# Kernel tuning notes

Hardware: AMD Instinct MI355X
Metric: run time of the kernel (lower is better)

The kernel has to match this reference:

```python
import jax, jax.numpy as jnp
import numpy as np

D_MODEL = 2048
D_FFN = 8192
RANK = 16
MOD_SCALE = 0.1
EPS = 1e-6


def setup_inputs() -> dict:
    key = jax.random.key(0)
    ks = jax.random.split(key, 8)
    B, S = 2, 2048
    init_scale = 0.01
    return {
        'hidden_states': jax.random.normal(ks[0], (B, S, D_MODEL), jnp.float32),
        'attn_output': jax.random.normal(ks[1], (B, S, D_MODEL), jnp.float32),
        'A': jax.random.normal(ks[2], (D_MODEL, RANK), jnp.float32) * (init_scale / np.sqrt(D_MODEL)),
        'Bmat': jax.random.normal(ks[3], (RANK, D_FFN), jnp.float32) * (init_scale / np.sqrt(RANK)),
        'W_in': jax.random.normal(ks[4], (D_FFN, D_MODEL), jnp.float32) * 0.02,  # gate_proj.weight
        'W_up': jax.random.normal(ks[5], (D_FFN, D_MODEL), jnp.float32) * 0.02,  # up_proj.weight
        'W_down': jax.random.normal(ks[6], (D_MODEL, D_FFN), jnp.float32) * 0.02,  # down_proj.weight
        'gamma': jnp.ones((D_MODEL,), jnp.float32),  # post_attention_layernorm (RMSNorm) weight
    }


def _rmsnorm(x, gamma):
    var = jnp.mean(x * x, axis=-1, keepdims=True)
    return x * jax.lax.rsqrt(var + EPS) * gamma


def reference(hidden_states, attn_output, A, Bmat, W_in, W_up, W_down, gamma):
    residual = hidden_states
    # Neuro-plastic modulation: [B,S,r]
    modulation = MOD_SCALE * jnp.tanh(jnp.einsum('bsd,dr->bsr', attn_output, A))
    # NPT applies post-attn norm to the residual (not residual+attn)
    h = _rmsnorm(residual, gamma)  # [B,S,d_model]
    # Fused per-token weight delta: delta_w^T @ h == B^T ((A^T h) * mod)
    hA = jnp.einsum('bsd,dr->bsr', h, A)  # [B,S,r]
    delta_out = jnp.einsum('bsr,rf->bsf', hA * modulation, Bmat)  # [B,S,d_ffn]
    gate = jax.nn.silu(jnp.einsum('bsd,fd->bsf', h, W_in) + delta_out)
    up = jnp.einsum('bsd,fd->bsf', h, W_up)
    out = jnp.einsum('bsf,df->bsd', gate * up, W_down)
    return residual + out
```

## Files before the change

kernel.cpp:

```cpp
#include <hip/hip_runtime.h>
#include <cstdint>
#include <cstddef>

#define D_MODEL 2048
#define D_FFN   8192
#define RANK    16
#define EPS     1e-6f
#define MOD_SCALE 0.1f

typedef float    f32x4 __attribute__((ext_vector_type(4)));
typedef _Float16 half8 __attribute__((ext_vector_type(8)));
typedef _Float16 half4 __attribute__((ext_vector_type(4)));

__device__ __forceinline__ void async_load16(const void* g, void* l) {
  __builtin_amdgcn_global_load_lds(
      (const __attribute__((address_space(1))) uint32_t*)g,
      (__attribute__((address_space(3))) uint32_t*)l,
      16, 0, 0);
}

__device__ __forceinline__ void stage_tile(const _Float16* __restrict__ gbase,
                                           size_t stride, _Float16* lds, int tid) {
  #pragma unroll
  for (int j = 0; j < 4; ++j) {
    int idx = j * 256 + tid;
    int row = idx >> 3;
    int c   = (idx & 7) ^ (row & 7);
    async_load16(gbase + (size_t)row * stride + c * 8, &lds[idx * 8]);
  }
}

__device__ __forceinline__ half8 frag_read(const _Float16* lds, int r, int c) {
  return *(const half8*)&lds[r * 64 + ((c ^ (r & 7)) * 8)];
}

__global__ __launch_bounds__(256) void convert_f32_f16(
    const float* __restrict__ s, _Float16* __restrict__ d)
{
  size_t i = ((size_t)blockIdx.x * 256 + threadIdx.x) * 8;
  f32x4 a = *(const f32x4*)(s + i);
  f32x4 b = *(const f32x4*)(s + i + 4);
  half8 h;
  #pragma unroll
  for (int j = 0; j < 4; ++j) { h[j] = (_Float16)a[j]; h[4+j] = (_Float16)b[j]; }
  *(half8*)(d + i) = h;
}

__global__ __launch_bounds__(256) void prep_kernel(
    const float* __restrict__ hs, const float* __restrict__ attn,
    const float* __restrict__ Amat, const float* __restrict__ gamma,
    _Float16* __restrict__ h16, float* __restrict__ cmat)
{
  const int token = blockIdx.x;
  const int tid   = threadIdx.x;
  const int lane  = tid & 63;
  const int wv    = tid >> 6;
  const size_t tb = (size_t)token * D_MODEL;
  const int base  = tid * 8;

  f32x4 x0 = *(const f32x4*)(hs + tb + base);
  f32x4 x1 = *(const f32x4*)(hs + tb + base + 4);
  f32x4 a0 = *(const f32x4*)(attn + tb + base);
  f32x4 a1 = *(const f32x4*)(attn + tb + base + 4);

  float ss = 0.f;
  #pragma unroll
  for (int j = 0; j < 4; ++j) ss += x0[j]*x0[j] + x1[j]*x1[j];
  #pragma unroll
  for (int off = 32; off > 0; off >>= 1) ss += __shfl_xor(ss, off, 64);

  __shared__ float red[4];
  __shared__ float redp[4][RANK];
  __shared__ float redh[4][RANK];
  if (lane == 0) red[wv] = ss;
  __syncthreads();
  const float tot = red[0] + red[1] + red[2] + red[3];
  const float rms = rsqrtf(tot * (1.0f / D_MODEL) + EPS);

  f32x4 g0 = *(const f32x4*)(gamma + base);
  f32x4 g1 = *(const f32x4*)(gamma + base + 4);
  float hv[8], av[8];
  #pragma unroll
  for (int j = 0; j < 4; ++j) {
    hv[j]   = x0[j] * rms * g0[j];
    hv[4+j] = x1[j] * rms * g1[j];
    av[j]   = a0[j];
    av[4+j] = a1[j];
  }
  half8 hh;
  #pragma unroll
  for (int j = 0; j < 8; ++j) hh[j] = (_Float16)hv[j];
  *(half8*)(h16 + tb + base) = hh;

  float pa[RANK], ph[RANK];
  #pragma unroll
  for (int r = 0; r < RANK; ++r) { pa[r] = 0.f; ph[r] = 0.f; }
  #pragma unroll
  for (int e = 0; e < 8; ++e) {
    const f32x4* Ar = (const f32x4*)(Amat + (size_t)(base + e) * RANK);
    #pragma unroll
    for (int q = 0; q < 4; ++q) {
      f32x4 ar = Ar[q];
      #pragma unroll
      for (int j = 0; j < 4; ++j) {
        pa[q*4+j] += av[e] * ar[j];
        ph[q*4+j] += hv[e] * ar[j];
      }
    }
  }
  #pragma unroll
  for (int r = 0; r < RANK; ++r) {
    #pragma unroll
    for (int off = 32; off > 0; off >>= 1) {
      pa[r] += __shfl_xor(pa[r], off, 64);
      ph[r] += __shfl_xor(ph[r], off, 64);
    }
  }
  if (lane == 0) {
    #pragma unroll
    for (int r = 0; r < RANK; ++r) { redp[wv][r] = pa[r]; redh[wv][r] = ph[r]; }
  }
  __syncthreads();
  if (tid < RANK) {
    float sp = redp[0][tid] + redp[1][tid] + redp[2][tid] + redp[3][tid];
    float sh = redh[0][tid] + redh[1][tid] + redh[2][tid] + redh[3][tid];
    cmat[(size_t)token * RANK + tid] = sh * (MOD_SCALE * tanhf(sp));
  }
}

__global__ __launch_bounds__(256, 2) void gemm_gateup(
    const _Float16* __restrict__ h16,
    const _Float16* __restrict__ Wg16, const _Float16* __restrict__ Wu16,
    const float* __restrict__ cmat, const float* __restrict__ Bmat,
    _Float16* __restrict__ tmat)
{
  __shared__ __align__(16) _Float16 sA [128*64];
  __shared__ __align__(16) _Float16 sB1[128*64];
  __shared__ __align__(16) _Float16 sB2[128*64];

  const int tid  = threadIdx.x;
  const int lane = tid & 63;
  const int wv   = tid >> 6;
  const int wm   = (wv >> 1) * 64;
  const int wn   = (wv & 1) * 64;
  const int lr   = lane & 15;
  const int quad = lane >> 4;
  const int gm0  = blockIdx.y * 128;
  const int gn0  = blockIdx.x * 128;

  f32x4 accG[4][4], accU[4][4];
  #pragma unroll
  for (int i = 0; i < 4; ++i)
    #pragma unroll
    for (int j = 0; j < 4; ++j) {
      f32x4 z = {0.f, 0.f, 0.f, 0.f};
      accG[i][j] = z; accU[i][j] = z;
    }

  for (int kt = 0; kt < D_MODEL / 64; ++kt) {
    __syncthreads();
    stage_tile(h16  + (size_t)gm0 * D_MODEL + kt * 64, D_MODEL, sA,  tid);
    stage_tile(Wg16 + (size_t)gn0 * D_MODEL + kt * 64, D_MODEL, sB1, tid);
    stage_tile(Wu16 + (size_t)gn0 * D_MODEL + kt * 64, D_MODEL, sB2, tid);
    __syncthreads();
    #pragma unroll
    for (int ks = 0; ks < 2; ++ks) {
      const int ck = ks * 4 + quad;
      half8 af[4], bg[4], bu[4];
      #pragma unroll
      for (int im = 0; im < 4; ++im)
        af[im] = frag_read(sA, wm + im * 16 + lr, ck);
      #pragma unroll
      for (int in = 0; in < 4; ++in) {
        bg[in] = frag_read(sB1, wn + in * 16 + lr, ck);
        bu[in] = frag_read(sB2, wn + in * 16 + lr, ck);
      }
      #pragma unroll
      for (int im = 0; im < 4; ++im)
        #pragma unroll
        for (int in = 0; in < 4; ++in) {
          accG[im][in] = __builtin_amdgcn_mfma_f32_16x16x32_f16(af[im], bg[in], accG[im][in], 0, 0, 0);
          accU[im][in] = __builtin_amdgcn_mfma_f32_16x16x32_f16(af[im], bu[in], accU[im][in], 0, 0, 0);
        }
    }
  }

  __syncthreads();
  #pragma unroll
  for (int i = 0; i < 16; ++i) {
    int idx = i * 256 + tid;
    int m = idx >> 5, kk = idx & 31;
    sA[idx]  = (kk < RANK) ? (_Float16)cmat[(size_t)(gm0 + m) * RANK + kk] : (_Float16)0.0f;
    sB1[idx] = (kk < RANK) ? (_Float16)Bmat[(size_t)kk * D_FFN + gn0 + m]  : (_Float16)0.0f;
  }
  __syncthreads();
  {
    const int ko = quad * 8;
    half8 af[4], bd[4];
    #pragma unroll
    for (int im = 0; im < 4; ++im)
      af[im] = *(const half8*)&sA[(wm + im * 16 + lr) * 32 + ko];
    #pragma unroll
    for (int in = 0; in < 4; ++in)
      bd[in] = *(const half8*)&sB1[(wn + in * 16 + lr) * 32 + ko];
    #pragma unroll
    for (int im = 0; im < 4; ++im)
      #pragma unroll
      for (int in = 0; in < 4; ++in)
        accG[im][in] = __builtin_amdgcn_mfma_f32_16x16x32_f16(af[im], bd[in], accG[im][in], 0, 0, 0);
  }

  #pragma unroll
  for (int im = 0; im < 4; ++im)
    #pragma unroll
    for (int in = 0; in < 4; ++in) {
      const int growb = gm0 + wm + im * 16 + quad * 4;
      const int gcol  = gn0 + wn + in * 16 + lr;
      #pragma unroll
      for (int r = 0; r < 4; ++r) {
        float g = accG[im][in][r];
        float u = accU[im][in][r];
        float s = g / (1.0f + __expf(-g));
        tmat[(size_t)(growb + r) * D_FFN + gcol] = (_Float16)(s * u);
      }
    }
}

__global__ __launch_bounds__(256, 2) void gemm_down(
    const _Float16* __restrict__ tmat, const _Float16* __restrict__ Wd16,
    const float* __restrict__ hs, float* __restrict__ out)
{
  __shared__ __align__(16) _Float16 sA[128*64];
  __shared__ __align__(16) _Float16 sB[128*64];

  const int tid  = threadIdx.x;
  const int lane = tid & 63;
  const int wv   = tid >> 6;
  const int wm   = (wv >> 1) * 64;
  const int wn   = (wv & 1) * 64;
  const int lr   = lane & 15;
  const int quad = lane >> 4;
  const int gm0  = blockIdx.y * 128;
  const int gn0  = blockIdx.x * 128;

  f32x4 acc[4][4];
  #pragma unroll
  for (int i = 0; i < 4; ++i)
    #pragma unroll
    for (int j = 0; j < 4; ++j) {
      f32x4 z = {0.f, 0.f, 0.f, 0.f};
      acc[i][j] = z;
    }

  for (int kt = 0; kt < D_FFN / 64; ++kt) {
    __syncthreads();
    stage_tile(tmat + (size_t)gm0 * D_FFN + kt * 64, D_FFN, sA, tid);
    stage_tile(Wd16 + (size_t)gn0 * D_FFN + kt * 64, D_FFN, sB, tid);
    __syncthreads();
    #pragma unroll
    for (int ks = 0; ks < 2; ++ks) {
      const int ck = ks * 4 + quad;
      half8 af[4], bf_[4];
      #pragma unroll
      for (int im = 0; im < 4; ++im)
        af[im] = frag_read(sA, wm + im * 16 + lr, ck);
      #pragma unroll
      for (int in = 0; in < 4; ++in)
        bf_[in] = frag_read(sB, wn + in * 16 + lr, ck);
      #pragma unroll
      for (int im = 0; im < 4; ++im)
        #pragma unroll
        for (int in = 0; in < 4; ++in)
          acc[im][in] = __builtin_amdgcn_mfma_f32_16x16x32_f16(af[im], bf_[in], acc[im][in], 0, 0, 0);
    }
  }

  #pragma unroll
  for (int im = 0; im < 4; ++im)
    #pragma unroll
    for (int in = 0; in < 4; ++in) {
      const int growb = gm0 + wm + im * 16 + quad * 4;
      const int gcol  = gn0 + wn + in * 16 + lr;
      #pragma unroll
      for (int r = 0; r < 4; ++r) {
        size_t o = (size_t)(growb + r) * D_MODEL + gcol;
        out[o] = hs[o] + acc[im][in][r];
      }
    }
}

extern "C" void kernel_launch(void* const* d_in, const int* in_sizes, int n_in,
                              void* d_out, int out_size, void* d_ws, size_t ws_size,
                              hipStream_t stream) {
  const float* hs    = (const float*)d_in[0];
  const float* attn  = (const float*)d_in[1];
  const float* Amat  = (const float*)d_in[2];
  const float* Bmat  = (const float*)d_in[3];
  const float* Wg    = (const float*)d_in[4];
  const float* Wu    = (const float*)d_in[5];
  const float* Wd    = (const float*)d_in[6];
  const float* gamma = (const float*)d_in[7];
  float* out = (float*)d_out;

  const int M = in_sizes[0] / D_MODEL;
  const size_t WD = (size_t)D_FFN * D_MODEL;

  char* ws = (char*)d_ws;
  _Float16* h16  = (_Float16*)ws;
  float*    cmat = (float*)(ws + (size_t)M * D_MODEL * 2);
  _Float16* tmat = (_Float16*)(ws + (size_t)M * D_MODEL * 2 + (size_t)M * RANK * 4);
  _Float16* wbuf = tmat + (size_t)M * D_FFN;
  _Float16* Wg16 = wbuf;
  _Float16* Wu16 = wbuf + WD;
  _Float16* Wd16 = wbuf;

  const int convBlocks = (int)(WD / (256 * 8));

  prep_kernel<<<M, 256, 0, stream>>>(hs, attn, Amat, gamma, h16, cmat);
  convert_f32_f16<<<convBlocks, 256, 0, stream>>>(Wg, Wg16);
  convert_f32_f16<<<convBlocks, 256, 0, stream>>>(Wu, Wu16);
  gemm_gateup<<<dim3(D_FFN / 128, M / 128), 256, 0, stream>>>(h16, Wg16, Wu16, cmat, Bmat, tmat);
  convert_f32_f16<<<convBlocks, 256, 0, stream>>>(Wd, Wd16);
  gemm_down<<<dim3(D_MODEL / 128, M / 128), 256, 0, stream>>>(tmat, Wd16, hs, out);
}
```

Measured before the change: 776.9 us.

## Switch both GEMMs to 32x32x16 MFMA tiles and vectorize low-rank epilogue staging

Replaces the 16x16x32 MFMA fragments with 32x32x16 instructions in both the gate/up and down GEMMs, so each wave issues fewer, larger matrix ops and reads fewer LDS fragments per k-step. The low-rank delta correction is restaged with vector loads into a compact K=16 layout instead of a zero-padded K=32 one. The down GEMM's occupancy hint rises to 3 blocks per CU. When the workspace is large enough, the W_down conversion gets its own buffer and is issued before the gate/up GEMM rather than reusing the gate buffer afterwards. The risks are register pressure from 16-wide accumulators and a changed output row mapping in the epilogue.

```diff
diff --git a/kernel.cpp b/kernel.cpp
--- a/kernel.cpp
+++ b/kernel.cpp
@@ -8,9 +8,9 @@
 #define EPS     1e-6f
 #define MOD_SCALE 0.1f
 
-typedef float    f32x4 __attribute__((ext_vector_type(4)));
-typedef _Float16 half8 __attribute__((ext_vector_type(8)));
-typedef _Float16 half4 __attribute__((ext_vector_type(4)));
+typedef float    f32x4  __attribute__((ext_vector_type(4)));
+typedef float    f32x16 __attribute__((ext_vector_type(16)));
+typedef _Float16 half8  __attribute__((ext_vector_type(8)));
 
 __device__ __forceinline__ void async_load16(const void* g, void* l) {
   __builtin_amdgcn_global_load_lds(
@@ -143,18 +143,18 @@
   const int wv   = tid >> 6;
   const int wm   = (wv >> 1) * 64;
   const int wn   = (wv & 1) * 64;
-  const int lr   = lane & 15;
-  const int quad = lane >> 4;
+  const int l31  = lane & 31;
+  const int h32  = lane >> 5;
   const int gm0  = blockIdx.y * 128;
   const int gn0  = blockIdx.x * 128;
 
-  f32x4 accG[4][4], accU[4][4];
-  #pragma unroll
-  for (int i = 0; i < 4; ++i)
-    #pragma unroll
-    for (int j = 0; j < 4; ++j) {
-      f32x4 z = {0.f, 0.f, 0.f, 0.f};
-      accG[i][j] = z; accU[i][j] = z;
+  f32x16 accG[2][2], accU[2][2];
+  #pragma unroll
+  for (int i = 0; i < 2; ++i)
+    #pragma unroll
+    for (int j = 0; j < 2; ++j) {
+      accG[i][j] = (f32x16)(0.0f);
+      accU[i][j] = (f32x16)(0.0f);
     }
 
   for (int kt = 0; kt < D_MODEL / 64; ++kt) {
@@ -164,69 +164,81 @@
     stage_tile(Wu16 + (size_t)gn0 * D_MODEL + kt * 64, D_MODEL, sB2, tid);
     __syncthreads();
     #pragma unroll
-    for (int ks = 0; ks < 2; ++ks) {
-      const int ck = ks * 4 + quad;
-      half8 af[4], bg[4], bu[4];
-      #pragma unroll
-      for (int im = 0; im < 4; ++im)
-        af[im] = frag_read(sA, wm + im * 16 + lr, ck);
-      #pragma unroll
-      for (int in = 0; in < 4; ++in) {
-        bg[in] = frag_read(sB1, wn + in * 16 + lr, ck);
-        bu[in] = frag_read(sB2, wn + in * 16 + lr, ck);
+    for (int kc = 0; kc < 4; ++kc) {
+      const int ck = kc * 2 + h32;
+      half8 af[2], bg[2], bu[2];
+      #pragma unroll
+      for (int im = 0; im < 2; ++im)
+        af[im] = frag_read(sA, wm + im * 32 + l31, ck);
+      #pragma unroll
+      for (int in = 0; in < 2; ++in) {
+        bg[in] = frag_read(sB1, wn + in * 32 + l31, ck);
+        bu[in] = frag_read(sB2, wn + in * 32 + l31, ck);
       }
       #pragma unroll
-      for (int im = 0; im < 4; ++im)
+      for (int im = 0; im < 2; ++im)
         #pragma unroll
-        for (int in = 0; in < 4; ++in) {
-          accG[im][in] = __builtin_amdgcn_mfma_f32_16x16x32_f16(af[im], bg[in], accG[im][in], 0, 0, 0);
-          accU[im][in] = __builtin_amdgcn_mfma_f32_16x16x32_f16(af[im], bu[in], accU[im][in], 0, 0, 0);
+        for (int in = 0; in < 2; ++in) {
+          accG[im][in] = __builtin_amdgcn_mfma_f32_32x32x16_f16(af[im], bg[in], accG[im][in], 0, 0, 0);
+          accU[im][in] = __builtin_amdgcn_mfma_f32_32x32x16_f16(af[im], bu[in], accU[im][in], 0, 0, 0);
         }
     }
   }
 
-  __syncthreads();
-  #pragma unroll
-  for (int i = 0; i < 16; ++i) {
-    int idx = i * 256 + tid;
-    int m = idx >> 5, kk = idx & 31;
-    sA[idx]  = (kk < RANK) ? (_Float16)cmat[(size_t)(gm0 + m) * RANK + kk] : (_Float16)0.0f;
-    sB1[idx] = (kk < RANK) ? (_Float16)Bmat[(size_t)kk * D_FFN + gn0 + m]  : (_Float16)0.0f;
-  }
+  _Float16* sC = sA;
+  _Float16* sD = sA + 128 * 16;
   __syncthreads();
   {
-    const int ko = quad * 8;
-    half8 af[4], bd[4];
-    #pragma unroll
-    for (int im = 0; im < 4; ++im)
-      af[im] = *(const half8*)&sA[(wm + im * 16 + lr) * 32 + ko];
-    #pragma unroll
-    for (int in = 0; in < 4; ++in)
-      bd[in] = *(const half8*)&sB1[(wn + in * 16 + lr) * 32 + ko];
-    #pragma unroll
-    for (int im = 0; im < 4; ++im)
-      #pragma unroll
-      for (int in = 0; in < 4; ++in)
-        accG[im][in] = __builtin_amdgcn_mfma_f32_16x16x32_f16(af[im], bd[in], accG[im][in], 0, 0, 0);
-  }
-
-  #pragma unroll
-  for (int im = 0; im < 4; ++im)
-    #pragma unroll
-    for (int in = 0; in < 4; ++in) {
-      const int growb = gm0 + wm + im * 16 + quad * 4;
-      const int gcol  = gn0 + wn + in * 16 + lr;
-      #pragma unroll
-      for (int r = 0; r < 4; ++r) {
+    int m = tid >> 1, k0 = (tid & 1) * 8;
+    f32x4 c0 = *(const f32x4*)(cmat + (size_t)(gm0 + m) * RANK + k0);
+    f32x4 c1 = *(const f32x4*)(cmat + (size_t)(gm0 + m) * RANK + k0 + 4);
+    half8 hc;
+    #pragma unroll
+    for (int j = 0; j < 4; ++j) { hc[j] = (_Float16)c0[j]; hc[4+j] = (_Float16)c1[j]; }
+    *(half8*)&sC[m * 16 + k0] = hc;
+
+    int kk = tid >> 4, n0 = (tid & 15) * 8;
+    f32x4 b0 = *(const f32x4*)(Bmat + (size_t)kk * D_FFN + gn0 + n0);
+    f32x4 b1 = *(const f32x4*)(Bmat + (size_t)kk * D_FFN + gn0 + n0 + 4);
+    #pragma unroll
+    for (int j = 0; j < 4; ++j) {
+      sD[(n0 + j) * 16 + kk]     = (_Float16)b0[j];
+      sD[(n0 + 4 + j) * 16 + kk] = (_Float16)b1[j];
+    }
+  }
+  __syncthreads();
+  {
+    half8 af[2], bd[2];
+    #pragma unroll
+    for (int im = 0; im < 2; ++im)
+      af[im] = *(const half8*)&sC[(wm + im * 32 + l31) * 16 + h32 * 8];
+    #pragma unroll
+    for (int in = 0; in < 2; ++in)
+      bd[in] = *(const half8*)&sD[(wn + in * 32 + l31) * 16 + h32 * 8];
+    #pragma unroll
+    for (int im = 0; im < 2; ++im)
+      #pragma unroll
+      for (int in = 0; in < 2; ++in)
+        accG[im][in] = __builtin_amdgcn_mfma_f32_32x32x16_f16(af[im], bd[in], accG[im][in], 0, 0, 0);
+  }
+
+  #pragma unroll
+  for (int im = 0; im < 2; ++im)
+    #pragma unroll
+    for (int in = 0; in < 2; ++in) {
+      const int col = gn0 + wn + in * 32 + l31;
+      #pragma unroll
+      for (int r = 0; r < 16; ++r) {
+        const int row = gm0 + wm + im * 32 + (r & 3) + 8 * (r >> 2) + 4 * h32;
         float g = accG[im][in][r];
         float u = accU[im][in][r];
         float s = g / (1.0f + __expf(-g));
-        tmat[(size_t)(growb + r) * D_FFN + gcol] = (_Float16)(s * u);
+        tmat[(size_t)row * D_FFN + col] = (_Float16)(s * u);
       }
     }
 }
 
-__global__ __launch_bounds__(256, 2) void gemm_down(
+__global__ __launch_bounds__(256, 3) void gemm_down(
     const _Float16* __restrict__ tmat, const _Float16* __restrict__ Wd16,
     const float* __restrict__ hs, float* __restrict__ out)
 {
@@ -238,19 +250,17 @@
   const int wv   = tid >> 6;
   const int wm   = (wv >> 1) * 64;
   const int wn   = (wv & 1) * 64;
-  const int lr   = lane & 15;
-  const int quad = lane >> 4;
+  const int l31  = lane & 31;
+  const int h32  = lane >> 5;
   const int gm0  = blockIdx.y * 128;
   const int gn0  = blockIdx.x * 128;
 
-  f32x4 acc[4][4];
-  #pragma unroll
-  for (int i = 0; i < 4; ++i)
-    #pragma unroll
-    for (int j = 0; j < 4; ++j) {
-      f32x4 z = {0.f, 0.f, 0.f, 0.f};
-      acc[i][j] = z;
-    }
+  f32x16 acc[2][2];
+  #pragma unroll
+  for (int i = 0; i < 2; ++i)
+    #pragma unroll
+    for (int j = 0; j < 2; ++j)
+      acc[i][j] = (f32x16)(0.0f);
 
   for (int kt = 0; kt < D_FFN / 64; ++kt) {
     __syncthreads();
@@ -258,32 +268,32 @@
     stage_tile(Wd16 + (size_t)gn0 * D_FFN + kt * 64, D_FFN, sB, tid);
     __syncthreads();
     #pragma unroll
-    for (int ks = 0; ks < 2; ++ks) {
-      const int ck = ks * 4 + quad;
-      half8 af[4], bf_[4];
-      #pragma unroll
-      for (int im = 0; im < 4; ++im)
-        af[im] = frag_read(sA, wm + im * 16 + lr, ck);
-      #pragma unroll
-      for (int in = 0; in < 4; ++in)
-        bf_[in] = frag_read(sB, wn + in * 16 + lr, ck);
-      #pragma unroll
-      for (int im = 0; im < 4; ++im)
+    for (int kc = 0; kc < 4; ++kc) {
+      const int ck = kc * 2 + h32;
+      half8 af[2], bf_[2];
+      #pragma unroll
+      for (int im = 0; im < 2; ++im)
+        af[im] = frag_read(sA, wm + im * 32 + l31, ck);
+      #pragma unroll
+      for (int in = 0; in < 2; ++in)
+        bf_[in] = frag_read(sB, wn + in * 32 + l31, ck);
+      #pragma unroll
+      for (int im = 0; im < 2; ++im)
         #pragma unroll
-        for (int in = 0; in < 4; ++in)
-          acc[im][in] = __builtin_amdgcn_mfma_f32_16x16x32_f16(af[im], bf_[in], acc[im][in], 0, 0, 0);
-    }
-  }
-
-  #pragma unroll
-  for (int im = 0; im < 4; ++im)
-    #pragma unroll
-    for (int in = 0; in < 4; ++in) {
-      const int growb = gm0 + wm + im * 16 + quad * 4;
-      const int gcol  = gn0 + wn + in * 16 + lr;
-      #pragma unroll
-      for (int r = 0; r < 4; ++r) {
-        size_t o = (size_t)(growb + r) * D_MODEL + gcol;
+        for (int in = 0; in < 2; ++in)
+          acc[im][in] = __builtin_amdgcn_mfma_f32_32x32x16_f16(af[im], bf_[in], acc[im][in], 0, 0, 0);
+    }
+  }
+
+  #pragma unroll
+  for (int im = 0; im < 2; ++im)
+    #pragma unroll
+    for (int in = 0; in < 2; ++in) {
+      const int col = gn0 + wn + in * 32 + l31;
+      #pragma unroll
+      for (int r = 0; r < 16; ++r) {
+        const int row = gm0 + wm + im * 32 + (r & 3) + 8 * (r >> 2) + 4 * h32;
+        size_t o = (size_t)row * D_MODEL + col;
         out[o] = hs[o] + acc[im][in][r];
       }
     }
@@ -312,14 +322,19 @@
   _Float16* wbuf = tmat + (size_t)M * D_FFN;
   _Float16* Wg16 = wbuf;
   _Float16* Wu16 = wbuf + WD;
-  _Float16* Wd16 = wbuf;
+
+  const size_t base_bytes = (size_t)M * D_MODEL * 2 + (size_t)M * RANK * 4
+                          + (size_t)M * D_FFN * 2 + 2 * WD * 2;
+  const bool sep_wd = (ws_size >= base_bytes + WD * 2);
+  _Float16* Wd16 = sep_wd ? (wbuf + 2 * WD) : wbuf;
 
   const int convBlocks = (int)(WD / (256 * 8));
 
   prep_kernel<<<M, 256, 0, stream>>>(hs, attn, Amat, gamma, h16, cmat);
   convert_f32_f16<<<convBlocks, 256, 0, stream>>>(Wg, Wg16);
   convert_f32_f16<<<convBlocks, 256, 0, stream>>>(Wu, Wu16);
+  if (sep_wd) convert_f32_f16<<<convBlocks, 256, 0, stream>>>(Wd, Wd16);
   gemm_gateup<<<dim3(D_FFN / 128, M / 128), 256, 0, stream>>>(h16, Wg16, Wu16, cmat, Bmat, tmat);
-  convert_f32_f16<<<convBlocks, 256, 0, stream>>>(Wd, Wd16);
+  if (!sep_wd) convert_f32_f16<<<convBlocks, 256, 0, stream>>>(Wd, Wd16);
   gemm_down<<<dim3(D_MODEL / 128, M / 128), 256, 0, stream>>>(tmat, Wd16, hs, out);
 }
```

After: 807.8 us. 4.0% more time.
